# Performance work log

Hardware: AMD Instinct MI355X
Metric: run time of the kernel (lower is better)

Reference implementation:

```python
import jax, jax.numpy as jnp
import numpy as np

B, N, M, D, H = 2, 256, 64, 768, 12
HD = D // H  # head dim 64


def setup_inputs() -> dict:
    key = jax.random.key(0)
    ks = jax.random.split(key, 8)
    s = 0.02
    return {
        "x": jax.random.normal(ks[0], (B, N, D), jnp.float32),
        "sim_embeddings": jax.random.normal(ks[1], (B, N, M, D), jnp.float32),
        "Wq": jax.random.normal(ks[2], (D, D), jnp.float32) * s,
        "bq": jnp.zeros((D,), jnp.float32),
        "Wkv": jax.random.normal(ks[3], (D, 2 * D), jnp.float32) * s,
        "bkv": jnp.zeros((2 * D,), jnp.float32),
        "Wp": jax.random.normal(ks[4], (D, D), jnp.float32) * s,
        "bp": jnp.zeros((D,), jnp.float32),
    }


def reference(x, sim_embeddings, Wq, bq, Wkv, bkv, Wp, bp):
    # x: (B,N,D); sim_embeddings: (B,N,M,D)
    b, n, d = x.shape
    m = sim_embeddings.shape[2]
    scale = HD ** -0.5

    q = (x @ Wq + bq).reshape(b, n, H, HD).transpose(0, 2, 1, 3)  # (B,H,N,hd)

    kv_x = x @ Wkv + bkv                       # (B,N,2D)
    k_x, v_x = jnp.split(kv_x, 2, axis=-1)
    k_x = k_x.reshape(b, n, H, HD).transpose(0, 2, 1, 3)  # (B,H,N,hd) shared-global K
    v_x = v_x.reshape(b, n, H, HD).transpose(0, 2, 1, 3)

    kv_s = sim_embeddings @ Wkv + bkv          # (B,N,M,2D)
    k_s, v_s = jnp.split(kv_s, 2, axis=-1)
    k_s = k_s.reshape(b, n, m, H, HD).transpose(0, 3, 1, 2, 4)  # (B,H,N,M,hd) per-query local K
    v_s = v_s.reshape(b, n, m, H, HD).transpose(0, 3, 1, 2, 4)

    # scores over concatenated [global N keys | local M keys] without expanding K to (B,N,N+M,D)
    sg = jnp.einsum('bhnd,bhkd->bhnk', q, k_x) * scale   # (B,H,N,N)
    sl = jnp.einsum('bhnd,bhnmd->bhnm', q, k_s) * scale  # (B,H,N,M)
    attn = jax.nn.softmax(jnp.concatenate([sg, sl], axis=-1), axis=-1)
    ag, al = attn[..., :n], attn[..., n:]

    out = (jnp.einsum('bhnk,bhkd->bhnd', ag, v_x)
           + jnp.einsum('bhnm,bhnmd->bhnd', al, v_s))   # (B,H,N,hd)
    out = out.transpose(0, 2, 1, 3).reshape(b, n, d)
    return out @ Wp + bp
```

## Files before the change

### kernel.cpp

```cpp
#include <hip/hip_runtime.h>
#include <stdint.h>

#define DEV_INLINE __device__ __forceinline__

typedef __bf16 bf16x8 __attribute__((ext_vector_type(8)));
typedef float f32x4 __attribute__((ext_vector_type(4)));

typedef const __attribute__((address_space(1))) void* gas_ptr;
typedef __attribute__((address_space(3))) void* las_ptr;

DEV_INLINE unsigned short f2bf(float f) {
    union { __bf16 h; unsigned short u; } v;
    v.h = (__bf16)f;
    return v.u;
}

template <int N> DEV_INLINE void waitcnt_vm() {
    asm volatile("s_waitcnt vmcnt(%0)" :: "n"(N) : "memory");
}
DEV_INLINE void hard_barrier() {
    __builtin_amdgcn_sched_barrier(0);
    __builtin_amdgcn_s_barrier();
    __builtin_amdgcn_sched_barrier(0);
}
DEV_INLINE void lds_barrier() {
    __builtin_amdgcn_sched_barrier(0);
    asm volatile("s_waitcnt lgkmcnt(0)" ::: "memory");
    __builtin_amdgcn_s_barrier();
    __builtin_amdgcn_sched_barrier(0);
}

__global__ __launch_bounds__(256)
void prep_cast_kernel(const float* __restrict__ x, unsigned short* __restrict__ xb,
                      const float* __restrict__ Wkv, unsigned short* __restrict__ wkvb,
                      const float* __restrict__ bq, const float* __restrict__ bkv,
                      float* __restrict__ bias1, float* __restrict__ zbuf) {
    int bid = blockIdx.x;
    if (bid < 1536) {
        const float* s; unsigned short* d; long i;
        if (bid < 384) { s = x;   d = xb;   i = (long)bid * 256 + threadIdx.x; }
        else           { s = Wkv; d = wkvb; i = (long)(bid - 384) * 256 + threadIdx.x; }
        float4 a = ((const float4*)s)[i];
        ushort4 o;
        o.x = f2bf(a.x); o.y = f2bf(a.y); o.z = f2bf(a.z); o.w = f2bf(a.w);
        ((ushort4*)d)[i] = o;
    } else {
        int i = (bid - 1536) * 256 + threadIdx.x;
        if (i < 768) bias1[i] = bq[i];
        else if (i < 2304) bias1[i] = bkv[i - 768];
        else zbuf[i - 2304] = 0.f;
    }
}

__global__ void transpose3_kernel(const float* __restrict__ Wq,
                                  const float* __restrict__ Wkv,
                                  const float* __restrict__ Wp,
                                  unsigned short* __restrict__ w1t,
                                  unsigned short* __restrict__ wpt) {
    __shared__ float tl[64][65];
    int bx = blockIdx.x;
    const float* src; unsigned short* dst; int C;
    if (bx < 12)      { src = Wq;  dst = w1t;              C = 768; }
    else if (bx < 36) { src = Wkv; dst = w1t + 768L * 768; C = 1536; bx -= 12; }
    else              { src = Wp;  dst = wpt;              C = 768; bx -= 36; }
    int c0 = bx * 64, r0 = blockIdx.y * 64;
    int tx = threadIdx.x, ty = threadIdx.y;
    #pragma unroll
    for (int i = 0; i < 64; i += 16)
        tl[ty + i][tx] = src[(long)(r0 + ty + i) * C + c0 + tx];
    __syncthreads();
    #pragma unroll
    for (int i = 0; i < 64; i += 16)
        dst[(long)(c0 + ty + i) * 768 + r0 + tx] = f2bf(tl[tx][ty + i]);
}

template <int WM, int WN, int WAVES_M, bool G1E>
DEV_INLINE void gemm_body(const unsigned short* A, int lda,
                          const unsigned short* BT, int ldb,
                          const unsigned short* A2, int lda2,
                          const unsigned short* B2, int ldb2, int K1,
                          const float* bias, void* Cout, int ldc, int K,
                          const float* cin, int OUT, long obase, long tm, long tn,
                          unsigned short* As, unsigned short* Bs,
                          float* g1_qf, unsigned short* g1_qb,
                          unsigned short* g1_kxb, unsigned short* g1_vxT) {
    constexpr int TR = WAVES_M * WM * 16;
    constexpr int TC = (4 / WAVES_M) * WN * 16;
    constexpr int NL = TR / 32 + TC / 32;
    const int tid = threadIdx.x;
    const int w = tid >> 6, lane = tid & 63;
    const int lm = lane & 15, quad = lane >> 4;
    const int m_off = (w % WAVES_M) * WM * 16;
    const int n_off = (w / WAVES_M) * WN * 16;
    const int lrow8 = lane >> 3;
    const int lcol_sw = (((lane & 7) ^ lrow8) * 8);

    f32x4 acc[WM][WN];
    #pragma unroll
    for (int mi = 0; mi < WM; ++mi)
        #pragma unroll
        for (int ni = 0; ni < WN; ++ni) acc[mi][ni] = f32x4{0.f, 0.f, 0.f, 0.f};

    auto stage = [&](int k0, int pb) {
        const unsigned short* Ab; const unsigned short* Bb;
        int la, lb, kc;
        if (k0 < K1) { Ab = A;  Bb = BT; la = lda;  lb = ldb;  kc = k0; }
        else         { Ab = A2; Bb = B2; la = lda2; lb = ldb2; kc = k0 - K1; }
        unsigned short* Asb = As + pb * (TR * 64);
        unsigned short* Bsb = Bs + pb * (TC * 64);
        #pragma unroll
        for (int i = 0; i < TR / 32; ++i) {
            int rr = w * (TR / 4) + i * 8;
            const unsigned short* ga = Ab + (tm + rr + lrow8) * la + kc + lcol_sw;
            __builtin_amdgcn_global_load_lds((gas_ptr)ga, (las_ptr)(Asb + rr * 64), 16, 0, 0);
        }
        #pragma unroll
        for (int i = 0; i < TC / 32; ++i) {
            int rr = w * (TC / 4) + i * 8;
            const unsigned short* gb = Bb + (tn + rr + lrow8) * lb + kc + lcol_sw;
            __builtin_amdgcn_global_load_lds((gas_ptr)gb, (las_ptr)(Bsb + rr * 64), 16, 0, 0);
        }
    };

    stage(0, 0);
    const int nt = K >> 6;
    for (int t = 0; t < nt; ++t) {
        const int cur = t & 1;
        if (t + 1 < nt) {
            stage((t + 1) << 6, cur ^ 1);
            waitcnt_vm<NL>();
        } else {
            waitcnt_vm<0>();
        }
        hard_barrier();
        const unsigned short* Asb = As + cur * (TR * 64);
        const unsigned short* Bsb = Bs + cur * (TC * 64);
        #pragma unroll
        for (int kk = 0; kk < 2; ++kk) {
            bf16x8 af[WM], bfr[WN];
            #pragma unroll
            for (int mi = 0; mi < WM; ++mi) {
                int r = m_off + mi * 16 + lm;
                af[mi] = *(const bf16x8*)(Asb + r * 64 + (((kk * 4 + quad) ^ (r & 7)) * 8));
            }
            #pragma unroll
            for (int ni = 0; ni < WN; ++ni) {
                int r = n_off + ni * 16 + lm;
                bfr[ni] = *(const bf16x8*)(Bsb + r * 64 + (((kk * 4 + quad) ^ (r & 7)) * 8));
            }
            #pragma unroll
            for (int mi = 0; mi < WM; ++mi)
                #pragma unroll
                for (int ni = 0; ni < WN; ++ni)
                    acc[mi][ni] = __builtin_amdgcn_mfma_f32_16x16x32_bf16(
                        af[mi], bfr[ni], acc[mi][ni], 0, 0, 0);
        }
        hard_barrier();
    }

    #pragma unroll
    for (int mi = 0; mi < WM; ++mi) {
        #pragma unroll
        for (int ni = 0; ni < WN; ++ni) {
            long col = tn + n_off + ni * 16 + lm;
            float bv = bias[col];
            #pragma unroll
            for (int r = 0; r < 4; ++r) {
                long row = tm + m_off + mi * 16 + quad * 4 + r;
                float v = acc[mi][ni][r] + bv;
                if (G1E) {
                    if (col < 768) {
                        g1_qf[row * 768 + col] = v;
                        g1_qb[row * 768 + col] = f2bf(v);
                    } else if (col < 1536) {
                        g1_kxb[row * 768 + (col - 768)] = f2bf(v);
                    } else {
                        int j = (int)col - 1536, h = j >> 6, d = j & 63;
                        int bb = (int)row >> 8, nn = (int)row & 255;
                        g1_vxT[((long)(bb * 12 + h) * 64 + d) * 256 + nn] = f2bf(v);
                    }
                } else {
                    long idx = obase + row * ldc + col;
                    if (cin) v += cin[idx];
                    if (OUT == 0) ((float*)Cout)[idx] = v;
                    else ((unsigned short*)Cout)[idx] = f2bf(v);
                }
            }
        }
    }
}

template <int WM, int WN, int WAVES_M, bool G1E>
__global__ __launch_bounds__(256)
void gemm_bf16_kernel(const unsigned short* __restrict__ A, int lda,
                      const unsigned short* __restrict__ BT, int ldb,
                      const float* __restrict__ bias,
                      void* __restrict__ Cout, int ldc, int K,
                      const float* __restrict__ cin, int OUT,
                      long aZb, long aZh, long bZb, long bZh, long oZb, long oZh,
                      float* __restrict__ g1_qf, unsigned short* __restrict__ g1_qb,
                      unsigned short* __restrict__ g1_kxb,
                      unsigned short* __restrict__ g1_vxT) {
    constexpr int TR = WAVES_M * WM * 16;
    constexpr int TC = (4 / WAVES_M) * WN * 16;
    __shared__ unsigned short As[2 * TR * 64];
    __shared__ unsigned short Bs[2 * TC * 64];
    const int z = blockIdx.z, zb = z / 12, zh = z % 12;
    gemm_body<WM, WN, WAVES_M, G1E>(
        A + zb * aZb + zh * aZh, lda, BT + zb * bZb + zh * bZh, ldb,
        nullptr, 0, nullptr, 0, 1 << 30,
        bias, Cout, ldc, K, cin, OUT, zb * oZb + zh * oZh,
        (long)blockIdx.y * TR, (long)blockIdx.x * TC, As, Bs,
        g1_qf, g1_qb, g1_kxb, g1_vxT);
}

__global__ __launch_bounds__(256)
void gemm_qwsg_kernel(const unsigned short* __restrict__ qb,
                      const unsigned short* __restrict__ wkvb,
                      const unsigned short* __restrict__ kxb,
                      const float* __restrict__ zbuf,
                      unsigned short* __restrict__ qWb,
                      float* __restrict__ sgbuf) {
    __shared__ unsigned short As[2 * 64 * 64];
    __shared__ unsigned short Bs[2 * 64 * 64];
    int bid = blockIdx.x;
    if (bid < 1152) {
        int bx = bid % 12, by = (bid / 12) % 8, h = bid / 96;
        gemm_body<2, 2, 2, false>(
            qb + h * 64, 768, wkvb + h * 64, 1536,
            nullptr, 0, nullptr, 0, 1 << 30,
            zbuf, qWb, 768, 64, nullptr, 1, (long)h * 393216,
            (long)by * 64, (long)bx * 64, As, Bs,
            nullptr, nullptr, nullptr, nullptr);
    } else {
        int bid2 = bid - 1152;
        int bx = bid2 % 4, by = (bid2 / 4) % 4, z = bid2 / 16;
        int zb = z / 12, zh = z % 12;
        gemm_body<2, 2, 2, false>(
            qb + zb * 196608 + zh * 64, 768, kxb + zb * 196608 + zh * 64, 768,
            nullptr, 0, nullptr, 0, 1 << 30,
            zbuf, sgbuf, 256, 64, nullptr, 0,
            (long)zb * 786432 + (long)zh * 65536,
            (long)by * 64, (long)bx * 64, As, Bs,
            nullptr, nullptr, nullptr, nullptr);
    }
}

template <int WM, int WN, int WAVES_M>
__global__ __launch_bounds__(256)
void gemm_concat_kernel(const unsigned short* __restrict__ A, int lda, long aZb, long aZh,
                        const unsigned short* __restrict__ BT, int ldb, long bZb, long bZh,
                        const unsigned short* __restrict__ A2, int lda2, long a2Zb, long a2Zh,
                        const unsigned short* __restrict__ B2, int ldb2, long b2Zb, long b2Zh,
                        int K1, int K, const float* __restrict__ bias,
                        void* __restrict__ Cout, int ldc,
                        const float* __restrict__ cin, int OUT, long oZb, long oZh) {
    constexpr int TR = WAVES_M * WM * 16;
    constexpr int TC = (4 / WAVES_M) * WN * 16;
    __shared__ unsigned short As[2 * TR * 64];
    __shared__ unsigned short Bs[2 * TC * 64];
    const int z = blockIdx.z, zb = z / 12, zh = z % 12;
    gemm_body<WM, WN, WAVES_M, false>(
        A + zb * aZb + zh * aZh, lda, BT + zb * bZb + zh * bZh, ldb,
        A2 + zb * a2Zb + zh * a2Zh, lda2, B2 + zb * b2Zb + zh * b2Zh, ldb2, K1,
        bias, Cout, ldc, K, cin, OUT, zb * oZb + zh * oZh,
        (long)blockIdx.y * TR, (long)blockIdx.x * TC, As, Bs,
        nullptr, nullptr, nullptr, nullptr);
}

__global__ __launch_bounds__(512, 4)
void attn_fused_kernel(const float* __restrict__ sim,
                       const unsigned short* __restrict__ qWb,
                       const float* __restrict__ qf,
                       const float* __restrict__ bkv,
                       const float* __restrict__ sgbuf,
                       unsigned short* __restrict__ agb,
                       float* __restrict__ outg0,
                       unsigned short* __restrict__ simbar) {
    __shared__ unsigned short qw_s[12 * 784];
    __shared__ unsigned short sim_s[2][2][64 * 64];
    __shared__ float q_l[768];
    __shared__ float slb_s[12];
    __shared__ float scl[2][12][68];
    __shared__ float al_s[12][64];

    const int t = threadIdx.x;
    const int lane = t & 63, w = t >> 6;
    const int lm = lane & 15, quad = lane >> 4;
    const int g = w >> 2, wl = w & 3;
    const int tg = t & 255;
    const int n = blockIdx.x, b = blockIdx.y;
    const int n_ = b * 256 + n;
    const float* simn = sim + (long)n_ * 49152;

    {
        const int h = t >> 5, c0 = t & 31;
        if (h < 12) {
            const unsigned short* src = qWb + ((long)h * 512 + n_) * 768;
            #pragma unroll
            for (int j = 0; j < 3; ++j) {
                int ch = c0 + 32 * j;
                *(bf16x8*)(qw_s + h * 784 + ch * 8) = *(const bf16x8*)(src + ch * 8);
            }
        }
    }
    q_l[t] = qf[(long)n_ * 768 + t];
    if (t < 256) q_l[t + 512] = qf[(long)n_ * 768 + t + 512];

    const int r0 = tg >> 3, q8 = tg & 7, r1 = r0 + 32;
    const int kb = g * 6;
    float4 p0a, p0b, p1a, p1b;
    {
        const float* g0 = simn + r0 * 768 + kb * 64 + q8 * 8;
        p0a = *(const float4*)g0; p0b = *(const float4*)(g0 + 4);
        const float* g1 = simn + r1 * 768 + kb * 64 + q8 * 8;
        p1a = *(const float4*)g1; p1b = *(const float4*)(g1 + 4);
    }
    __syncthreads();
    if (t < 12) {
        float s = 0.f;
        #pragma unroll 8
        for (int d = 0; d < 64; ++d) s += q_l[t * 64 + d] * bkv[t * 64 + d];
        slb_s[t] = s;
    }

    f32x4 acc = {};
    #pragma unroll
    for (int cc = 0; cc < 6; ++cc) {
        const int k0 = (kb + cc) * 64;
        unsigned short* buf = sim_s[g][cc & 1];
        union { bf16x8 v; unsigned short u[8]; } pk;
        pk.u[0] = f2bf(p0a.x); pk.u[1] = f2bf(p0a.y);
        pk.u[2] = f2bf(p0a.z); pk.u[3] = f2bf(p0a.w);
        pk.u[4] = f2bf(p0b.x); pk.u[5] = f2bf(p0b.y);
        pk.u[6] = f2bf(p0b.z); pk.u[7] = f2bf(p0b.w);
        *(bf16x8*)(buf + r0 * 64 + ((q8 ^ (r0 & 7)) * 8)) = pk.v;
        pk.u[0] = f2bf(p1a.x); pk.u[1] = f2bf(p1a.y);
        pk.u[2] = f2bf(p1a.z); pk.u[3] = f2bf(p1a.w);
        pk.u[4] = f2bf(p1b.x); pk.u[5] = f2bf(p1b.y);
        pk.u[6] = f2bf(p1b.z); pk.u[7] = f2bf(p1b.w);
        *(bf16x8*)(buf + r1 * 64 + ((q8 ^ (r1 & 7)) * 8)) = pk.v;
        if (cc < 5) {
            const float* g0 = simn + r0 * 768 + k0 + 64 + q8 * 8;
            p0a = *(const float4*)g0; p0b = *(const float4*)(g0 + 4);
            const float* g1 = simn + r1 * 768 + k0 + 64 + q8 * 8;
            p1a = *(const float4*)g1; p1b = *(const float4*)(g1 + 4);
        }
        lds_barrier();
        #pragma unroll
        for (int kk = 0; kk < 2; ++kk) {
            int r = wl * 16 + lm;
            bf16x8 af = *(const bf16x8*)(buf + r * 64 + (((kk * 4 + quad) ^ (r & 7)) * 8));
            bf16x8 bfr = *(const bf16x8*)(qw_s + lm * 784 + k0 + kk * 32 + quad * 8);
            acc = __builtin_amdgcn_mfma_f32_16x16x32_bf16(af, bfr, acc, 0, 0, 0);
        }
    }
    if (lm < 12) {
        #pragma unroll
        for (int r = 0; r < 4; ++r)
            scl[g][lm][wl * 16 + quad * 4 + r] = acc[r];
    }
    __syncthreads();

    if (w < 6) {
        #pragma unroll
        for (int i = 0; i < 2; ++i) {
            const int h = w * 2 + i;
            const float* sgr = sgbuf + (long)(b * 12 + h) * 65536 + (long)n * 256;
            float v0 = sgr[lane] * 0.125f, v1 = sgr[lane + 64] * 0.125f,
                  v2 = sgr[lane + 128] * 0.125f, v3 = sgr[lane + 192] * 0.125f;
            float v4 = (scl[0][h][lane] + scl[1][h][lane] + slb_s[h]) * 0.125f;
            float mx = fmaxf(fmaxf(fmaxf(v0, v1), fmaxf(v2, v3)), v4);
            #pragma unroll
            for (int off = 32; off > 0; off >>= 1) mx = fmaxf(mx, __shfl_xor(mx, off));
            float e0 = __expf(v0 - mx), e1 = __expf(v1 - mx), e2 = __expf(v2 - mx),
                  e3 = __expf(v3 - mx), e4 = __expf(v4 - mx);
            float s = e0 + e1 + e2 + e3 + e4;
            #pragma unroll
            for (int off = 32; off > 0; off >>= 1) s += __shfl_xor(s, off);
            float inv = __frcp_rn(s);
            unsigned short* agr = agb + (long)(b * 12 + h) * 65536 + (long)n * 256;
            agr[lane] = f2bf(e0 * inv); agr[lane + 64] = f2bf(e1 * inv);
            agr[lane + 128] = f2bf(e2 * inv); agr[lane + 192] = f2bf(e3 * inv);
            float al = e4 * inv;
            al_s[h][lane] = al;
            float am = al;
            #pragma unroll
            for (int off = 32; off > 0; off >>= 1) am += __shfl_xor(am, off);
            outg0[(long)n_ * 768 + h * 64 + lane] = am * bkv[768 + h * 64 + lane];
        }
    }
    __syncthreads();

    {
        float a[12];
        #pragma unroll
        for (int h = 0; h < 12; ++h) a[h] = 0.f;
        #pragma unroll 4
        for (int m = 0; m < 64; ++m) {
            float s = simn[(long)m * 768 + t];
            #pragma unroll
            for (int h = 0; h < 12; ++h) a[h] += al_s[h][m] * s;
        }
        #pragma unroll
        for (int h = 0; h < 12; ++h)
            simbar[((long)h * 512 + n_) * 768 + t] = f2bf(a[h]);
    }
    if (w < 4) {
        float a[12];
        #pragma unroll
        for (int h = 0; h < 12; ++h) a[h] = 0.f;
        #pragma unroll 4
        for (int m = 0; m < 64; ++m) {
            float s = simn[(long)m * 768 + 512 + t];
            #pragma unroll
            for (int h = 0; h < 12; ++h) a[h] += al_s[h][m] * s;
        }
        #pragma unroll
        for (int h = 0; h < 12; ++h)
            simbar[((long)h * 512 + n_) * 768 + 512 + t] = f2bf(a[h]);
    }
}


extern "C" void kernel_launch(void* const* d_in, const int* in_sizes, int n_in,
                              void* d_out, int out_size, void* d_ws, size_t ws_size,
                              hipStream_t stream) {
    const float* x   = (const float*)d_in[0];
    const float* sim = (const float*)d_in[1];
    const float* Wq  = (const float*)d_in[2];
    const float* bq  = (const float*)d_in[3];
    const float* Wkv = (const float*)d_in[4];
    const float* bkv = (const float*)d_in[5];
    const float* Wp  = (const float*)d_in[6];
    const float* bp  = (const float*)d_in[7];
    float* out = (float*)d_out;

    char* ws = (char*)d_ws;
    size_t off = 0;
    auto alloc = [&](size_t bytes) {
        char* p = ws + off;
        off += (bytes + 255) & ~(size_t)255;
        return p;
    };
    unsigned short* xb     = (unsigned short*)alloc(512UL * 768 * 2);
    unsigned short* w1t    = (unsigned short*)alloc(2304UL * 768 * 2);
    unsigned short* wkvb   = (unsigned short*)alloc(768UL * 1536 * 2);
    unsigned short* wpt    = (unsigned short*)alloc(768UL * 768 * 2);
    float*          qf     = (float*)alloc(512UL * 768 * 4);
    unsigned short* qb     = (unsigned short*)alloc(512UL * 768 * 2);
    unsigned short* kxb    = (unsigned short*)alloc(512UL * 768 * 2);
    unsigned short* vxT    = (unsigned short*)alloc(24UL * 64 * 256 * 2);
    unsigned short* qWb    = (unsigned short*)alloc(12UL * 512 * 768 * 2);
    float*          sgbuf  = (float*)alloc(24UL * 65536 * 4);
    unsigned short* agb    = (unsigned short*)alloc(24UL * 65536 * 2);
    float*          outg0  = (float*)alloc(512UL * 768 * 4);
    unsigned short* simbar = (unsigned short*)alloc(12UL * 512 * 768 * 2);
    unsigned short* attnb  = (unsigned short*)alloc(512UL * 768 * 2);
    float*          bias1  = (float*)alloc(2304UL * 4);
    float*          zbuf   = (float*)alloc(768UL * 4);

    prep_cast_kernel<<<1548, 256, 0, stream>>>(x, xb, Wkv, wkvb, bq, bkv, bias1, zbuf);
    transpose3_kernel<<<dim3(48, 12), dim3(64, 16), 0, stream>>>(Wq, Wkv, Wp, w1t, wpt);

    gemm_bf16_kernel<1, 2, 2, true><<<dim3(36, 16, 1), 256, 0, stream>>>(
        xb, 768, w1t, 768, bias1, nullptr, 768, 768, nullptr, 0,
        0, 0, 0, 0, 0, 0, qf, qb, kxb, vxT);

    gemm_qwsg_kernel<<<1536, 256, 0, stream>>>(qb, wkvb, kxb, zbuf, qWb, sgbuf);

    attn_fused_kernel<<<dim3(256, 2), 512, 0, stream>>>(
        sim, qWb, qf, bkv, sgbuf, agb, outg0, simbar);

    gemm_concat_kernel<1, 1, 2><<<dim3(2, 8, 24), 256, 0, stream>>>(
        simbar, 768, 196608, 393216,
        w1t + 1536L * 768, 768, 0, 49152,
        agb, 256, 786432, 65536,
        vxT, 256, 196608, 16384,
        768, 1024, zbuf, attnb, 768, outg0, 1, 196608, 64);

    gemm_bf16_kernel<1, 1, 2, false><<<dim3(24, 16, 1), 256, 0, stream>>>(
        attnb, 768, wpt, 768, bp, out, 768, 768, nullptr, 0,
        0, 0, 0, 0, 0, 0, nullptr, nullptr, nullptr, nullptr);
}
```

Measured before the change: 236.1 us.

## Split fused attention kernel into local-score and softmax/weighted-sum kernels

The single 512-thread fused attention kernel (512 blocks) is split in two. The first kernel computes partial local scores per half of the feature dimension (1024 blocks) and writes them to a workspace buffer. The second (1536 blocks) does the softmax and the weighted sum of the sim embeddings, with each block handling a 256-column slice. The goal is more parallelism and better load balance across CUs, and ending the idle waves in the old final phase. In exchange, each column-group block recomputes the softmax, the sim tensor is read twice from memory, and there is an extra launch plus a global round trip for the partial scores.

```diff
diff --git a/kernel.cpp b/kernel.cpp
--- a/kernel.cpp
+++ b/kernel.cpp
@@ -268,122 +268,129 @@
         nullptr, nullptr, nullptr, nullptr);
 }
 
-__global__ __launch_bounds__(512, 4)
-void attn_fused_kernel(const float* __restrict__ sim,
-                       const unsigned short* __restrict__ qWb,
-                       const float* __restrict__ qf,
-                       const float* __restrict__ bkv,
-                       const float* __restrict__ sgbuf,
-                       unsigned short* __restrict__ agb,
-                       float* __restrict__ outg0,
-                       unsigned short* __restrict__ simbar) {
-    __shared__ unsigned short qw_s[12 * 784];
-    __shared__ unsigned short sim_s[2][2][64 * 64];
-    __shared__ float q_l[768];
-    __shared__ float slb_s[12];
-    __shared__ float scl[2][12][68];
-    __shared__ float al_s[12][64];
-
+__global__ __launch_bounds__(256)
+void slpart_kernel(const float* __restrict__ sim,
+                   const unsigned short* __restrict__ qWb,
+                   float* __restrict__ sclp) {
+    __shared__ unsigned short qw_s[16 * 392];
+    __shared__ unsigned short ss[2][64 * 64];
     const int t = threadIdx.x;
-    const int lane = t & 63, w = t >> 6;
+    const int lane = t & 63, wl = t >> 6;
     const int lm = lane & 15, quad = lane >> 4;
-    const int g = w >> 2, wl = w & 3;
-    const int tg = t & 255;
-    const int n = blockIdx.x, b = blockIdx.y;
-    const int n_ = b * 256 + n;
-    const float* simn = sim + (long)n_ * 49152;
-
-    {
-        const int h = t >> 5, c0 = t & 31;
-        if (h < 12) {
-            const unsigned short* src = qWb + ((long)h * 512 + n_) * 768;
-            #pragma unroll
-            for (int j = 0; j < 3; ++j) {
-                int ch = c0 + 32 * j;
-                *(bf16x8*)(qw_s + h * 784 + ch * 8) = *(const bf16x8*)(src + ch * 8);
-            }
-        }
-    }
-    q_l[t] = qf[(long)n_ * 768 + t];
-    if (t < 256) q_l[t + 512] = qf[(long)n_ * 768 + t + 512];
-
-    const int r0 = tg >> 3, q8 = tg & 7, r1 = r0 + 32;
-    const int kb = g * 6;
-    float4 p0a, p0b, p1a, p1b;
-    {
-        const float* g0 = simn + r0 * 768 + kb * 64 + q8 * 8;
-        p0a = *(const float4*)g0; p0b = *(const float4*)(g0 + 4);
-        const float* g1 = simn + r1 * 768 + kb * 64 + q8 * 8;
-        p1a = *(const float4*)g1; p1b = *(const float4*)(g1 + 4);
+    const int n_ = blockIdx.x, half = blockIdx.y;
+    const int kb = half * 384;
+    const float* simn = sim + (long)n_ * 49152 + kb;
+
+    for (int idx = t; idx < 576; idx += 256) {
+        int h = idx / 48, c = idx % 48;
+        *(bf16x8*)(qw_s + h * 392 + c * 8) =
+            *(const bf16x8*)(qWb + ((long)h * 512 + n_) * 768 + kb + c * 8);
+    }
+
+    const int r0 = t >> 3, q8 = t & 7, r1 = r0 + 32;
+    float4 a0[2], b0[2], a1[2], b1[2];
+    #pragma unroll
+    for (int s = 0; s < 2; ++s) {
+        const float* g0 = simn + r0 * 768 + s * 64 + q8 * 8;
+        a0[s] = *(const float4*)g0; b0[s] = *(const float4*)(g0 + 4);
+        const float* g1 = simn + r1 * 768 + s * 64 + q8 * 8;
+        a1[s] = *(const float4*)g1; b1[s] = *(const float4*)(g1 + 4);
     }
     __syncthreads();
-    if (t < 12) {
-        float s = 0.f;
-        #pragma unroll 8
-        for (int d = 0; d < 64; ++d) s += q_l[t * 64 + d] * bkv[t * 64 + d];
-        slb_s[t] = s;
-    }
 
     f32x4 acc = {};
     #pragma unroll
-    for (int cc = 0; cc < 6; ++cc) {
-        const int k0 = (kb + cc) * 64;
-        unsigned short* buf = sim_s[g][cc & 1];
+    for (int c = 0; c < 6; ++c) {
+        const int s = c & 1;
+        unsigned short* buf = ss[s];
         union { bf16x8 v; unsigned short u[8]; } pk;
-        pk.u[0] = f2bf(p0a.x); pk.u[1] = f2bf(p0a.y);
-        pk.u[2] = f2bf(p0a.z); pk.u[3] = f2bf(p0a.w);
-        pk.u[4] = f2bf(p0b.x); pk.u[5] = f2bf(p0b.y);
-        pk.u[6] = f2bf(p0b.z); pk.u[7] = f2bf(p0b.w);
+        pk.u[0] = f2bf(a0[s].x); pk.u[1] = f2bf(a0[s].y);
+        pk.u[2] = f2bf(a0[s].z); pk.u[3] = f2bf(a0[s].w);
+        pk.u[4] = f2bf(b0[s].x); pk.u[5] = f2bf(b0[s].y);
+        pk.u[6] = f2bf(b0[s].z); pk.u[7] = f2bf(b0[s].w);
         *(bf16x8*)(buf + r0 * 64 + ((q8 ^ (r0 & 7)) * 8)) = pk.v;
-        pk.u[0] = f2bf(p1a.x); pk.u[1] = f2bf(p1a.y);
-        pk.u[2] = f2bf(p1a.z); pk.u[3] = f2bf(p1a.w);
-        pk.u[4] = f2bf(p1b.x); pk.u[5] = f2bf(p1b.y);
-        pk.u[6] = f2bf(p1b.z); pk.u[7] = f2bf(p1b.w);
+        pk.u[0] = f2bf(a1[s].x); pk.u[1] = f2bf(a1[s].y);
+        pk.u[2] = f2bf(a1[s].z); pk.u[3] = f2bf(a1[s].w);
+        pk.u[4] = f2bf(b1[s].x); pk.u[5] = f2bf(b1[s].y);
+        pk.u[6] = f2bf(b1[s].z); pk.u[7] = f2bf(b1[s].w);
         *(bf16x8*)(buf + r1 * 64 + ((q8 ^ (r1 & 7)) * 8)) = pk.v;
-        if (cc < 5) {
-            const float* g0 = simn + r0 * 768 + k0 + 64 + q8 * 8;
-            p0a = *(const float4*)g0; p0b = *(const float4*)(g0 + 4);
-            const float* g1 = simn + r1 * 768 + k0 + 64 + q8 * 8;
-            p1a = *(const float4*)g1; p1b = *(const float4*)(g1 + 4);
+        if (c < 4) {
+            const float* g0 = simn + r0 * 768 + (c + 2) * 64 + q8 * 8;
+            a0[s] = *(const float4*)g0; b0[s] = *(const float4*)(g0 + 4);
+            const float* g1 = simn + r1 * 768 + (c + 2) * 64 + q8 * 8;
+            a1[s] = *(const float4*)g1; b1[s] = *(const float4*)(g1 + 4);
         }
         lds_barrier();
         #pragma unroll
         for (int kk = 0; kk < 2; ++kk) {
             int r = wl * 16 + lm;
             bf16x8 af = *(const bf16x8*)(buf + r * 64 + (((kk * 4 + quad) ^ (r & 7)) * 8));
-            bf16x8 bfr = *(const bf16x8*)(qw_s + lm * 784 + k0 + kk * 32 + quad * 8);
+            bf16x8 bfr = *(const bf16x8*)(qw_s + lm * 392 + c * 64 + kk * 32 + quad * 8);
             acc = __builtin_amdgcn_mfma_f32_16x16x32_bf16(af, bfr, acc, 0, 0, 0);
         }
     }
     if (lm < 12) {
-        #pragma unroll
-        for (int r = 0; r < 4; ++r)
-            scl[g][lm][wl * 16 + quad * 4 + r] = acc[r];
+        float* dst = sclp + ((long)(n_ * 2 + half) * 12 + lm) * 64 + wl * 16 + quad * 4;
+        #pragma unroll
+        for (int r = 0; r < 4; ++r) dst[r] = acc[r];
+    }
+}
+
+__global__ __launch_bounds__(256)
+void attn2_kernel(const float* __restrict__ sim,
+                  const float* __restrict__ qf,
+                  const float* __restrict__ bkv,
+                  const float* __restrict__ sclp,
+                  const float* __restrict__ sgbuf,
+                  unsigned short* __restrict__ agb,
+                  float* __restrict__ outg0,
+                  unsigned short* __restrict__ simbar) {
+    __shared__ float slb_s[12];
+    __shared__ float al_s[12][64];
+    const int t = threadIdx.x;
+    const int lane = t & 63, w = t >> 6;
+    const int n_ = blockIdx.x, cg = blockIdx.y;
+    const int b = n_ >> 8, n = n_ & 255;
+    const float* simn = sim + (long)n_ * 49152;
+
+    {
+        float p0 = qf[(long)n_ * 768 + t] * bkv[t];
+        float p1 = qf[(long)n_ * 768 + t + 256] * bkv[t + 256];
+        float p2 = qf[(long)n_ * 768 + t + 512] * bkv[t + 512];
+        #pragma unroll
+        for (int off = 32; off > 0; off >>= 1) {
+            p0 += __shfl_xor(p0, off);
+            p1 += __shfl_xor(p1, off);
+            p2 += __shfl_xor(p2, off);
+        }
+        if (lane == 0) { slb_s[w] = p0; slb_s[w + 4] = p1; slb_s[w + 8] = p2; }
     }
     __syncthreads();
 
-    if (w < 6) {
-        #pragma unroll
-        for (int i = 0; i < 2; ++i) {
-            const int h = w * 2 + i;
-            const float* sgr = sgbuf + (long)(b * 12 + h) * 65536 + (long)n * 256;
-            float v0 = sgr[lane] * 0.125f, v1 = sgr[lane + 64] * 0.125f,
-                  v2 = sgr[lane + 128] * 0.125f, v3 = sgr[lane + 192] * 0.125f;
-            float v4 = (scl[0][h][lane] + scl[1][h][lane] + slb_s[h]) * 0.125f;
-            float mx = fmaxf(fmaxf(fmaxf(v0, v1), fmaxf(v2, v3)), v4);
-            #pragma unroll
-            for (int off = 32; off > 0; off >>= 1) mx = fmaxf(mx, __shfl_xor(mx, off));
-            float e0 = __expf(v0 - mx), e1 = __expf(v1 - mx), e2 = __expf(v2 - mx),
-                  e3 = __expf(v3 - mx), e4 = __expf(v4 - mx);
-            float s = e0 + e1 + e2 + e3 + e4;
-            #pragma unroll
-            for (int off = 32; off > 0; off >>= 1) s += __shfl_xor(s, off);
-            float inv = __frcp_rn(s);
+    #pragma unroll
+    for (int i = 0; i < 3; ++i) {
+        const int h = w * 3 + i;
+        const float* sgr = sgbuf + (long)(b * 12 + h) * 65536 + (long)n * 256;
+        float v0 = sgr[lane] * 0.125f, v1 = sgr[lane + 64] * 0.125f,
+              v2 = sgr[lane + 128] * 0.125f, v3 = sgr[lane + 192] * 0.125f;
+        float v4 = (sclp[((long)(n_ * 2) * 12 + h) * 64 + lane]
+                  + sclp[((long)(n_ * 2 + 1) * 12 + h) * 64 + lane]
+                  + slb_s[h]) * 0.125f;
+        float mx = fmaxf(fmaxf(fmaxf(v0, v1), fmaxf(v2, v3)), v4);
+        #pragma unroll
+        for (int off = 32; off > 0; off >>= 1) mx = fmaxf(mx, __shfl_xor(mx, off));
+        float e0 = __expf(v0 - mx), e1 = __expf(v1 - mx), e2 = __expf(v2 - mx),
+              e3 = __expf(v3 - mx), e4 = __expf(v4 - mx);
+        float s = e0 + e1 + e2 + e3 + e4;
+        #pragma unroll
+        for (int off = 32; off > 0; off >>= 1) s += __shfl_xor(s, off);
+        float inv = __frcp_rn(s);
+        float al = e4 * inv;
+        al_s[h][lane] = al;
+        if (cg == 0) {
             unsigned short* agr = agb + (long)(b * 12 + h) * 65536 + (long)n * 256;
             agr[lane] = f2bf(e0 * inv); agr[lane + 64] = f2bf(e1 * inv);
             agr[lane + 128] = f2bf(e2 * inv); agr[lane + 192] = f2bf(e3 * inv);
-            float al = e4 * inv;
-            al_s[h][lane] = al;
             float am = al;
             #pragma unroll
             for (int off = 32; off > 0; off >>= 1) am += __shfl_xor(am, off);
@@ -392,34 +399,19 @@
     }
     __syncthreads();
 
-    {
-        float a[12];
-        #pragma unroll
-        for (int h = 0; h < 12; ++h) a[h] = 0.f;
-        #pragma unroll 4
-        for (int m = 0; m < 64; ++m) {
-            float s = simn[(long)m * 768 + t];
-            #pragma unroll
-            for (int h = 0; h < 12; ++h) a[h] += al_s[h][m] * s;
-        }
-        #pragma unroll
-        for (int h = 0; h < 12; ++h)
-            simbar[((long)h * 512 + n_) * 768 + t] = f2bf(a[h]);
-    }
-    if (w < 4) {
-        float a[12];
-        #pragma unroll
-        for (int h = 0; h < 12; ++h) a[h] = 0.f;
-        #pragma unroll 4
-        for (int m = 0; m < 64; ++m) {
-            float s = simn[(long)m * 768 + 512 + t];
-            #pragma unroll
-            for (int h = 0; h < 12; ++h) a[h] += al_s[h][m] * s;
-        }
-        #pragma unroll
-        for (int h = 0; h < 12; ++h)
-            simbar[((long)h * 512 + n_) * 768 + 512 + t] = f2bf(a[h]);
-    }
+    const int c = cg * 256 + t;
+    float a[12];
+    #pragma unroll
+    for (int h = 0; h < 12; ++h) a[h] = 0.f;
+    #pragma unroll 4
+    for (int m = 0; m < 64; ++m) {
+        float s = simn[(long)m * 768 + c];
+        #pragma unroll
+        for (int h = 0; h < 12; ++h) a[h] += al_s[h][m] * s;
+    }
+    #pragma unroll
+    for (int h = 0; h < 12; ++h)
+        simbar[((long)h * 512 + n_) * 768 + c] = f2bf(a[h]);
 }
 
 
@@ -455,6 +447,7 @@
     float*          sgbuf  = (float*)alloc(24UL * 65536 * 4);
     unsigned short* agb    = (unsigned short*)alloc(24UL * 65536 * 2);
     float*          outg0  = (float*)alloc(512UL * 768 * 4);
+    float*          sclp   = (float*)alloc(512UL * 2 * 12 * 64 * 4);
     unsigned short* simbar = (unsigned short*)alloc(12UL * 512 * 768 * 2);
     unsigned short* attnb  = (unsigned short*)alloc(512UL * 768 * 2);
     float*          bias1  = (float*)alloc(2304UL * 4);
@@ -469,8 +462,10 @@
 
     gemm_qwsg_kernel<<<1536, 256, 0, stream>>>(qb, wkvb, kxb, zbuf, qWb, sgbuf);
 
-    attn_fused_kernel<<<dim3(256, 2), 512, 0, stream>>>(
-        sim, qWb, qf, bkv, sgbuf, agb, outg0, simbar);
+    slpart_kernel<<<dim3(512, 2), 256, 0, stream>>>(sim, qWb, sclp);
+
+    attn2_kernel<<<dim3(512, 3), 256, 0, stream>>>(
+        sim, qf, bkv, sclp, sgbuf, agb, outg0, simbar);
 
     gemm_concat_kernel<1, 1, 2><<<dim3(2, 8, 24), 256, 0, stream>>>(
         simbar, 768, 196608, 393216,
```

After: 243.1 us. +3.0%, slower.

## Stage whole sim tile in LDS, merge prep kernels, parallelize bias dot

Applied to the files above, without the earlier changes.

The attention kernel now loads all 12 column chunks of the per-query sim tile into a swizzled LDS buffer in one phase, then runs the MFMA score loop with no per-chunk barriers. Before, it double-buffered chunk by chunk with a barrier each step. The per-head q·bkv reduction now uses wave shuffles instead of 12 serial threads. The cast and transpose prep kernels are merged into one launch. The larger LDS footprint (~100KB) lowers occupancy, and the loss of load/compute overlap may offset the barrier savings.

```diff
diff --git a/kernel.cpp b/kernel.cpp
--- a/kernel.cpp
+++ b/kernel.cpp
@@ -23,55 +23,46 @@
     __builtin_amdgcn_s_barrier();
     __builtin_amdgcn_sched_barrier(0);
 }
-DEV_INLINE void lds_barrier() {
-    __builtin_amdgcn_sched_barrier(0);
-    asm volatile("s_waitcnt lgkmcnt(0)" ::: "memory");
-    __builtin_amdgcn_s_barrier();
-    __builtin_amdgcn_sched_barrier(0);
-}
 
 __global__ __launch_bounds__(256)
-void prep_cast_kernel(const float* __restrict__ x, unsigned short* __restrict__ xb,
-                      const float* __restrict__ Wkv, unsigned short* __restrict__ wkvb,
-                      const float* __restrict__ bq, const float* __restrict__ bkv,
-                      float* __restrict__ bias1, float* __restrict__ zbuf) {
-    int bid = blockIdx.x;
+void prep_all_kernel(const float* __restrict__ x, unsigned short* __restrict__ xb,
+                     const float* __restrict__ Wkv, unsigned short* __restrict__ wkvb,
+                     const float* __restrict__ bq, const float* __restrict__ bkv,
+                     float* __restrict__ bias1, float* __restrict__ zbuf,
+                     const float* __restrict__ Wq, const float* __restrict__ Wp,
+                     unsigned short* __restrict__ w1t, unsigned short* __restrict__ wpt) {
+    __shared__ float tl[64][65];
+    const int bid = blockIdx.x, t = threadIdx.x;
     if (bid < 1536) {
         const float* s; unsigned short* d; long i;
-        if (bid < 384) { s = x;   d = xb;   i = (long)bid * 256 + threadIdx.x; }
-        else           { s = Wkv; d = wkvb; i = (long)(bid - 384) * 256 + threadIdx.x; }
+        if (bid < 384) { s = x;   d = xb;   i = (long)bid * 256 + t; }
+        else           { s = Wkv; d = wkvb; i = (long)(bid - 384) * 256 + t; }
         float4 a = ((const float4*)s)[i];
         ushort4 o;
         o.x = f2bf(a.x); o.y = f2bf(a.y); o.z = f2bf(a.z); o.w = f2bf(a.w);
         ((ushort4*)d)[i] = o;
-    } else {
-        int i = (bid - 1536) * 256 + threadIdx.x;
+    } else if (bid < 1548) {
+        int i = (bid - 1536) * 256 + t;
         if (i < 768) bias1[i] = bq[i];
         else if (i < 2304) bias1[i] = bkv[i - 768];
         else zbuf[i - 2304] = 0.f;
-    }
-}
-
-__global__ void transpose3_kernel(const float* __restrict__ Wq,
-                                  const float* __restrict__ Wkv,
-                                  const float* __restrict__ Wp,
-                                  unsigned short* __restrict__ w1t,
-                                  unsigned short* __restrict__ wpt) {
-    __shared__ float tl[64][65];
-    int bx = blockIdx.x;
-    const float* src; unsigned short* dst; int C;
-    if (bx < 12)      { src = Wq;  dst = w1t;              C = 768; }
-    else if (bx < 36) { src = Wkv; dst = w1t + 768L * 768; C = 1536; bx -= 12; }
-    else              { src = Wp;  dst = wpt;              C = 768; bx -= 36; }
-    int c0 = bx * 64, r0 = blockIdx.y * 64;
-    int tx = threadIdx.x, ty = threadIdx.y;
-    #pragma unroll
-    for (int i = 0; i < 64; i += 16)
-        tl[ty + i][tx] = src[(long)(r0 + ty + i) * C + c0 + tx];
-    __syncthreads();
-    #pragma unroll
-    for (int i = 0; i < 64; i += 16)
-        dst[(long)(c0 + ty + i) * 768 + r0 + tx] = f2bf(tl[tx][ty + i]);
+    } else {
+        int tb = bid - 1548;
+        int bx = tb % 48, by = tb / 48;
+        const float* src; unsigned short* dst; int C;
+        if (bx < 12)      { src = Wq;  dst = w1t;              C = 768; }
+        else if (bx < 36) { src = Wkv; dst = w1t + 768L * 768; C = 1536; bx -= 12; }
+        else              { src = Wp;  dst = wpt;              C = 768; bx -= 36; }
+        int c0 = bx * 64, r0 = by * 64;
+        int tx = t & 63, ty = t >> 6;
+        #pragma unroll
+        for (int i = 0; i < 64; i += 4)
+            tl[ty + i][tx] = src[(long)(r0 + ty + i) * C + c0 + tx];
+        __syncthreads();
+        #pragma unroll
+        for (int i = 0; i < 64; i += 4)
+            dst[(long)(c0 + ty + i) * 768 + r0 + tx] = f2bf(tl[tx][ty + i]);
+    }
 }
 
 template <int WM, int WN, int WAVES_M, bool G1E>
@@ -268,97 +259,101 @@
         nullptr, nullptr, nullptr, nullptr);
 }
 
-__global__ __launch_bounds__(512, 4)
-void attn_fused_kernel(const float* __restrict__ sim,
-                       const unsigned short* __restrict__ qWb,
-                       const float* __restrict__ qf,
-                       const float* __restrict__ bkv,
-                       const float* __restrict__ sgbuf,
-                       unsigned short* __restrict__ agb,
-                       float* __restrict__ outg0,
-                       unsigned short* __restrict__ simbar) {
-    __shared__ unsigned short qw_s[12 * 784];
-    __shared__ unsigned short sim_s[2][2][64 * 64];
-    __shared__ float q_l[768];
-    __shared__ float slb_s[12];
+__global__ __launch_bounds__(512)
+void attn_mega_kernel(const float* __restrict__ sim,
+                      const unsigned short* __restrict__ qWb,
+                      const float* __restrict__ qf,
+                      const float* __restrict__ bkv,
+                      const float* __restrict__ sgbuf,
+                      unsigned short* __restrict__ agb,
+                      float* __restrict__ outg0,
+                      unsigned short* __restrict__ simbar) {
+    __shared__ unsigned short sim_s[12 * 64 * 64];
+    __shared__ unsigned short qw_s[16 * 784];
     __shared__ float scl[2][12][68];
     __shared__ float al_s[12][64];
+    __shared__ float slb_s[12];
 
     const int t = threadIdx.x;
     const int lane = t & 63, w = t >> 6;
     const int lm = lane & 15, quad = lane >> 4;
-    const int g = w >> 2, wl = w & 3;
-    const int tg = t & 255;
-    const int n = blockIdx.x, b = blockIdx.y;
-    const int n_ = b * 256 + n;
+    const int n_ = blockIdx.x;
+    const int b = n_ >> 8, n = n_ & 255;
     const float* simn = sim + (long)n_ * 49152;
 
+    #pragma unroll
+    for (int g3 = 0; g3 < 3; ++g3) {
+        float4 va[4], vb[4]; int dso[4];
+        #pragma unroll
+        for (int i = 0; i < 4; ++i) {
+            int j = t + 512 * (g3 * 4 + i);
+            int r = j / 96, rem = j - r * 96;
+            int c = rem >> 3, q8 = rem & 7;
+            const float* gp = simn + r * 768 + c * 64 + q8 * 8;
+            va[i] = *(const float4*)gp;
+            vb[i] = *(const float4*)(gp + 4);
+            dso[i] = c * 4096 + r * 64 + ((q8 ^ (r & 7)) * 8);
+        }
+        #pragma unroll
+        for (int i = 0; i < 4; ++i) {
+            union { bf16x8 v; unsigned short u[8]; } pk;
+            pk.u[0] = f2bf(va[i].x); pk.u[1] = f2bf(va[i].y);
+            pk.u[2] = f2bf(va[i].z); pk.u[3] = f2bf(va[i].w);
+            pk.u[4] = f2bf(vb[i].x); pk.u[5] = f2bf(vb[i].y);
+            pk.u[6] = f2bf(vb[i].z); pk.u[7] = f2bf(vb[i].w);
+            *(bf16x8*)(sim_s + dso[i]) = pk.v;
+        }
+    }
+
+    #pragma unroll
+    for (int rep = 0; rep < 2; ++rep) {
+        int i = t + rep * 512;
+        int h = i / 96, cc = i - h * 96;
+        *(bf16x8*)(qw_s + h * 784 + cc * 8) =
+            *(const bf16x8*)(qWb + ((long)h * 512 + n_) * 768 + cc * 8);
+    }
+    if (t < 128) {
+        int i = t + 1024;
+        int h = i / 96, cc = i - h * 96;
+        *(bf16x8*)(qw_s + h * 784 + cc * 8) =
+            *(const bf16x8*)(qWb + ((long)h * 512 + n_) * 768 + cc * 8);
+    }
+    if (t < 392) *(bf16x8*)(qw_s + 12 * 784 + t * 8) = bf16x8{};
+
+    if (t < 256) {
+        float p0 = qf[(long)n_ * 768 + t] * bkv[t];
+        float p1 = qf[(long)n_ * 768 + t + 256] * bkv[t + 256];
+        float p2 = qf[(long)n_ * 768 + t + 512] * bkv[t + 512];
+        #pragma unroll
+        for (int off = 32; off > 0; off >>= 1) {
+            p0 += __shfl_xor(p0, off);
+            p1 += __shfl_xor(p1, off);
+            p2 += __shfl_xor(p2, off);
+        }
+        if (lane == 0) { slb_s[w] = p0; slb_s[w + 4] = p1; slb_s[w + 8] = p2; }
+    }
+    __syncthreads();
+
     {
-        const int h = t >> 5, c0 = t & 31;
-        if (h < 12) {
-            const unsigned short* src = qWb + ((long)h * 512 + n_) * 768;
-            #pragma unroll
-            for (int j = 0; j < 3; ++j) {
-                int ch = c0 + 32 * j;
-                *(bf16x8*)(qw_s + h * 784 + ch * 8) = *(const bf16x8*)(src + ch * 8);
+        const int mb = w & 3, kh = w >> 2;
+        f32x4 acc = {};
+        const int r = mb * 16 + lm;
+        #pragma unroll
+        for (int cc = 0; cc < 6; ++cc) {
+            const int c = kh * 6 + cc;
+            #pragma unroll
+            for (int kk = 0; kk < 2; ++kk) {
+                bf16x8 af = *(const bf16x8*)(sim_s + c * 4096 + r * 64 +
+                                             (((kk * 4 + quad) ^ (r & 7)) * 8));
+                bf16x8 bfr = *(const bf16x8*)(qw_s + lm * 784 + c * 64 + kk * 32 + quad * 8);
+                acc = __builtin_amdgcn_mfma_f32_16x16x32_bf16(af, bfr, acc, 0, 0, 0);
             }
         }
-    }
-    q_l[t] = qf[(long)n_ * 768 + t];
-    if (t < 256) q_l[t + 512] = qf[(long)n_ * 768 + t + 512];
-
-    const int r0 = tg >> 3, q8 = tg & 7, r1 = r0 + 32;
-    const int kb = g * 6;
-    float4 p0a, p0b, p1a, p1b;
-    {
-        const float* g0 = simn + r0 * 768 + kb * 64 + q8 * 8;
-        p0a = *(const float4*)g0; p0b = *(const float4*)(g0 + 4);
-        const float* g1 = simn + r1 * 768 + kb * 64 + q8 * 8;
-        p1a = *(const float4*)g1; p1b = *(const float4*)(g1 + 4);
-    }
-    __syncthreads();
-    if (t < 12) {
-        float s = 0.f;
-        #pragma unroll 8
-        for (int d = 0; d < 64; ++d) s += q_l[t * 64 + d] * bkv[t * 64 + d];
-        slb_s[t] = s;
-    }
-
-    f32x4 acc = {};
-    #pragma unroll
-    for (int cc = 0; cc < 6; ++cc) {
-        const int k0 = (kb + cc) * 64;
-        unsigned short* buf = sim_s[g][cc & 1];
-        union { bf16x8 v; unsigned short u[8]; } pk;
-        pk.u[0] = f2bf(p0a.x); pk.u[1] = f2bf(p0a.y);
-        pk.u[2] = f2bf(p0a.z); pk.u[3] = f2bf(p0a.w);
-        pk.u[4] = f2bf(p0b.x); pk.u[5] = f2bf(p0b.y);
-        pk.u[6] = f2bf(p0b.z); pk.u[7] = f2bf(p0b.w);
-        *(bf16x8*)(buf + r0 * 64 + ((q8 ^ (r0 & 7)) * 8)) = pk.v;
-        pk.u[0] = f2bf(p1a.x); pk.u[1] = f2bf(p1a.y);
-        pk.u[2] = f2bf(p1a.z); pk.u[3] = f2bf(p1a.w);
-        pk.u[4] = f2bf(p1b.x); pk.u[5] = f2bf(p1b.y);
-        pk.u[6] = f2bf(p1b.z); pk.u[7] = f2bf(p1b.w);
-        *(bf16x8*)(buf + r1 * 64 + ((q8 ^ (r1 & 7)) * 8)) = pk.v;
-        if (cc < 5) {
-            const float* g0 = simn + r0 * 768 + k0 + 64 + q8 * 8;
-            p0a = *(const float4*)g0; p0b = *(const float4*)(g0 + 4);
-            const float* g1 = simn + r1 * 768 + k0 + 64 + q8 * 8;
-            p1a = *(const float4*)g1; p1b = *(const float4*)(g1 + 4);
-        }
-        lds_barrier();
-        #pragma unroll
-        for (int kk = 0; kk < 2; ++kk) {
-            int r = wl * 16 + lm;
-            bf16x8 af = *(const bf16x8*)(buf + r * 64 + (((kk * 4 + quad) ^ (r & 7)) * 8));
-            bf16x8 bfr = *(const bf16x8*)(qw_s + lm * 784 + k0 + kk * 32 + quad * 8);
-            acc = __builtin_amdgcn_mfma_f32_16x16x32_bf16(af, bfr, acc, 0, 0, 0);
-        }
-    }
-    if (lm < 12) {
-        #pragma unroll
-        for (int r = 0; r < 4; ++r)
-            scl[g][lm][wl * 16 + quad * 4 + r] = acc[r];
+        if (lm < 12) {
+            #pragma unroll
+            for (int r2 = 0; r2 < 4; ++r2)
+                scl[kh][lm][mb * 16 + quad * 4 + r2] = acc[r2];
+        }
     }
     __syncthreads();
 
@@ -406,7 +401,7 @@
         for (int h = 0; h < 12; ++h)
             simbar[((long)h * 512 + n_) * 768 + t] = f2bf(a[h]);
     }
-    if (w < 4) {
+    if (t < 256) {
         float a[12];
         #pragma unroll
         for (int h = 0; h < 12; ++h) a[h] = 0.f;
@@ -460,8 +455,8 @@
     float*          bias1  = (float*)alloc(2304UL * 4);
     float*          zbuf   = (float*)alloc(768UL * 4);
 
-    prep_cast_kernel<<<1548, 256, 0, stream>>>(x, xb, Wkv, wkvb, bq, bkv, bias1, zbuf);
-    transpose3_kernel<<<dim3(48, 12), dim3(64, 16), 0, stream>>>(Wq, Wkv, Wp, w1t, wpt);
+    prep_all_kernel<<<2124, 256, 0, stream>>>(
+        x, xb, Wkv, wkvb, bq, bkv, bias1, zbuf, Wq, Wp, w1t, wpt);
 
     gemm_bf16_kernel<1, 2, 2, true><<<dim3(36, 16, 1), 256, 0, stream>>>(
         xb, 768, w1t, 768, bias1, nullptr, 768, 768, nullptr, 0,
@@ -469,7 +464,7 @@
 
     gemm_qwsg_kernel<<<1536, 256, 0, stream>>>(qb, wkvb, kxb, zbuf, qWb, sgbuf);
 
-    attn_fused_kernel<<<dim3(256, 2), 512, 0, stream>>>(
+    attn_mega_kernel<<<512, 512, 0, stream>>>(
         sim, qWb, qf, bkv, sgbuf, agb, outg0, simbar);
 
     gemm_concat_kernel<1, 1, 2><<<dim3(2, 8, 24), 256, 0, stream>>>(
```

New measurement: 242.1 us. 2.6% more time.
